# Kernel tuning notes

Hardware: AMD Instinct MI355X
Metric: run time of the kernel (lower is better)

## Reference

```python
import jax, jax.numpy as jnp
import numpy as np

EPS = 1e-5  # torch group_norm default
GROUPS = 32


def _nin(t, W, b):
    # torch Nin: einsum('bchw,co->bowh') transposes spatial dims, then adds bias
    return jnp.einsum('bchw,co->bowh', t, W) + b


def setup_inputs() -> dict:
    key = jax.random.key(0)
    ks = jax.random.split(key, 9)
    B, C, N = 16, 512, 32
    x = jax.random.normal(ks[0], (B, C, N, N), jnp.float32)
    sc = 0.02
    Wq = jax.random.normal(ks[1], (C, C), jnp.float32) * sc
    Wk = jax.random.normal(ks[2], (C, C), jnp.float32) * sc
    Wv = jax.random.normal(ks[3], (C, C), jnp.float32) * sc
    Wn = jax.random.normal(ks[4], (C, C), jnp.float32) * sc
    bq = jnp.zeros((1, C, 1, 1), jnp.float32)
    bk = jnp.zeros((1, C, 1, 1), jnp.float32)
    bv = jnp.zeros((1, C, 1, 1), jnp.float32)
    bn = jnp.zeros((1, C, 1, 1), jnp.float32)
    return {"x": x, "Wq": Wq, "bq": bq, "Wk": Wk, "bk": bk,
            "Wv": Wv, "bv": bv, "Wn": Wn, "bn": bn}


def reference(x, Wq, bq, Wk, bk, Wv, bv, Wn, bn):
    B, C, H, W = x.shape
    # GroupNorm(32) with no affine params
    xg = x.reshape(B, GROUPS, -1)
    mu = xg.mean(-1, keepdims=True)
    var = xg.var(-1, keepdims=True)
    h = ((xg - mu) / jnp.sqrt(var + EPS)).reshape(B, C, H, W)
    # Nin projections -> spatially transposed (B, C, W, H)
    q = _nin(h, Wq, bq)
    k = _nin(h, Wk, bk)
    v = _nin(h, Wv, bv)
    # scores s[b,w1,w2,h1,h2] = sum_c q[b,c,w1,h1] k[b,c,w2,h2] * C^-0.5
    s = jnp.einsum('bcwh,bcWH->bwWhH', q, k) * (C ** -0.5)
    # softmax over flat (h1,h2) blocks exactly as the torch reshape does
    s = jax.nn.softmax(s.reshape(B, H, W, H * W), axis=-1).reshape(B, H, W, H, W)
    # torch.einsum('bHWHW, bcWH -> bcWH', w, v) takes the DIAGONAL over the
    # repeated H and W labels: diag[b,i,j] = s[b,i,j,i,j], then elementwise
    # scales v: out[b,c,w,h] = diag[b,h,w] * v[b,c,w,h]
    i = jnp.arange(H)
    j = jnp.arange(W)
    diag = s[:, i[:, None], j[None, :], i[:, None], j[None, :]]  # (B,H,W)
    h2 = v * jnp.swapaxes(diag, 1, 2)[:, None]  # (B,C,W,H)
    out = _nin(h2, Wn, bn)  # transposes back -> (B,C,H,W)
    return x + out
```

## Files before the change

kernel.cpp:

```cpp
#include <hip/hip_runtime.h>
#include <hip/hip_bf16.h>

typedef __attribute__((ext_vector_type(8))) short short8;
typedef __attribute__((ext_vector_type(4))) float floatx4;

#define MFMA16(a, b, c) __builtin_amdgcn_mfma_f32_16x16x32_bf16((a), (b), (c), 0, 0, 0)

__device__ __forceinline__ short f2bf(float f) {
    union { float f; unsigned u; } x; x.f = f;
    unsigned r = (x.u + 0x7fffu + ((x.u >> 16) & 1u)) >> 16;
    return (short)r;
}
__device__ __forceinline__ float bf2f(short s) {
    union { float f; unsigned u; } x; x.u = ((unsigned)(unsigned short)s) << 16;
    return x.f;
}

__device__ __forceinline__ void gl2lds16(const short* g, short* l) {
    void* gv = const_cast<short*>(g);
    __builtin_amdgcn_global_load_lds((__attribute__((address_space(1))) void*)gv,
                                     (__attribute__((address_space(3))) void*)l,
                                     16, 0, 0);
}

__global__ void transpose_w(const float* __restrict__ Wsrc, short* __restrict__ Wdst) {
    __shared__ float t[32][33];
    int o0 = blockIdx.x * 32, c0 = blockIdx.y * 32;
    int lx = threadIdx.x, ly = threadIdx.y;
    for (int i = ly; i < 32; i += 8) t[i][lx] = Wsrc[(size_t)(c0 + i) * 512 + o0 + lx];
    __syncthreads();
    for (int i = ly; i < 32; i += 8) Wdst[(size_t)(o0 + i) * 512 + c0 + lx] = f2bf(t[lx][i]);
}

__global__ __launch_bounds__(256) void groupnorm_k(const float* __restrict__ x,
                                                   short* __restrict__ hnt) {
    int b = blockIdx.x >> 5, g = blockIdx.x & 31;
    const float* xg = x + ((size_t)b * 512 + g * 16) * 1024;
    const float4* xg4 = (const float4*)xg;
    float s = 0.f, ss = 0.f;
    for (int i = threadIdx.x; i < 4096; i += 256) {
        float4 v = xg4[i];
        s  += v.x + v.y + v.z + v.w;
        ss += v.x * v.x + v.y * v.y + v.z * v.z + v.w * v.w;
    }
#pragma unroll
    for (int off = 32; off > 0; off >>= 1) {
        s  += __shfl_down(s,  off, 64);
        ss += __shfl_down(ss, off, 64);
    }
    __shared__ float red[8];
    int w = threadIdx.x >> 6;
    if ((threadIdx.x & 63) == 0) { red[w] = s; red[4 + w] = ss; }
    __syncthreads();
    float S  = red[0] + red[1] + red[2] + red[3];
    float SS = red[4] + red[5] + red[6] + red[7];
    float mean = S * (1.f / 16384.f);
    float var  = SS * (1.f / 16384.f) - mean * mean;
    float rstd = rsqrtf(var + 1e-5f);
    __shared__ __attribute__((aligned(16))) short tile[16 * 1026];
    for (int i = threadIdx.x; i < 4096; i += 256) {
        float4 v = xg4[i];
        int c = i >> 8, p = (i & 255) * 4;
        short* tp = tile + c * 1026 + p;
        tp[0] = f2bf((v.x - mean) * rstd);
        tp[1] = f2bf((v.y - mean) * rstd);
        tp[2] = f2bf((v.z - mean) * rstd);
        tp[3] = f2bf((v.w - mean) * rstd);
    }
    __syncthreads();
    for (int i = threadIdx.x; i < 2048; i += 256) {
        int p = i >> 1, half = i & 1;
        short8 v;
#pragma unroll
        for (int j = 0; j < 8; ++j) v[j] = tile[(half * 8 + j) * 1026 + p];
        *(short8*)(hnt + ((size_t)b * 1024 + p) * 512 + g * 16 + half * 8) = v;
    }
}

__global__ __launch_bounds__(256) void gemm_nt(const short* __restrict__ A, size_t a_bstride,
                                               const short* __restrict__ W,
                                               const float* __restrict__ bias,
                                               short* __restrict__ Out, size_t o_bstride,
                                               int permute) {
    const int tid = threadIdx.x;
    const int wv = tid >> 6, ln = tid & 63;
    const int m0 = blockIdx.x * 128, n0 = blockIdx.y * 128;
    const short* Ab = A + (size_t)blockIdx.z * a_bstride;
    short* Ob = Out + (size_t)blockIdx.z * o_bstride;

    __shared__ __attribute__((aligned(16))) short As[128 * 32];
    __shared__ __attribute__((aligned(16))) short Bs[128 * 32];

    floatx4 acc[4][4] = {};
    const int wm = (wv >> 1) * 64, wn = (wv & 1) * 64;
    const int fr = ln & 15, fq = ln >> 4;

    for (int kk = 0; kk < 512; kk += 32) {
        __syncthreads();
#pragma unroll
        for (int j = 0; j < 2; ++j) {
            int s = (wv * 2 + j) * 64 + ln;
            int r = s >> 2;
            int q = (s & 3) ^ ((r >> 1) & 3);
            short* lbase = As + (size_t)(wv * 2 + j) * 512;
            gl2lds16(Ab + (size_t)(m0 + r) * 512 + kk + q * 8, lbase);
            short* lbaseB = Bs + (size_t)(wv * 2 + j) * 512;
            gl2lds16(W + (size_t)(n0 + r) * 512 + kk + q * 8, lbaseB);
        }
        __syncthreads();
        short8 af[4], bfr[4];
#pragma unroll
        for (int t = 0; t < 4; ++t) {
            int ra = wm + t * 16 + fr;
            af[t]  = *(const short8*)(As + ra * 32 + ((fq ^ ((ra >> 1) & 3)) * 8));
            int rb = wn + t * 16 + fr;
            bfr[t] = *(const short8*)(Bs + rb * 32 + ((fq ^ ((rb >> 1) & 3)) * 8));
        }
#pragma unroll
        for (int mt = 0; mt < 4; ++mt)
#pragma unroll
            for (int nt = 0; nt < 4; ++nt)
                acc[mt][nt] = MFMA16(af[mt], bfr[nt], acc[mt][nt]);
    }
#pragma unroll
    for (int mt = 0; mt < 4; ++mt) {
#pragma unroll
        for (int nt = 0; nt < 4; ++nt) {
            int n = n0 + wn + nt * 16 + fr;
            float bvv = bias ? bias[n] : 0.0f;
#pragma unroll
            for (int r = 0; r < 4; ++r) {
                int m = m0 + wm + mt * 16 + fq * 4 + r;
                int mrow = permute ? ((m & 31) * 32 + (m >> 5)) : m;
                Ob[(size_t)mrow * 512 + n] = f2bf(acc[mt][nt][r] + bvv);
            }
        }
    }
}

__global__ __launch_bounds__(256) void attn_sm(const short* __restrict__ Qp,
                                               const short* __restrict__ Kp,
                                               float* __restrict__ Dm) {
    const int tid = threadIdx.x;
    const int wv = tid >> 6, ln = tid & 63;
    const int m0 = blockIdx.x * 128, n0 = blockIdx.y * 128, b = blockIdx.z;
    const short* Qb = Qp + (size_t)b * (1024 * 512);
    const short* Kb = Kp + (size_t)b * (1024 * 512);

    __shared__ __attribute__((aligned(16))) short As[128 * 32];
    __shared__ __attribute__((aligned(16))) short Bs[128 * 32];

    floatx4 acc[4][4] = {};
    const int wm = (wv >> 1) * 64, wn = (wv & 1) * 64;
    const int fr = ln & 15, fq = ln >> 4;

    for (int kk = 0; kk < 512; kk += 32) {
        __syncthreads();
#pragma unroll
        for (int j = 0; j < 2; ++j) {
            int s = (wv * 2 + j) * 64 + ln;
            int r = s >> 2;
            int q = (s & 3) ^ ((r >> 1) & 3);
            gl2lds16(Qb + (size_t)(m0 + r) * 512 + kk + q * 8, As + (size_t)(wv * 2 + j) * 512);
            gl2lds16(Kb + (size_t)(n0 + r) * 512 + kk + q * 8, Bs + (size_t)(wv * 2 + j) * 512);
        }
        __syncthreads();
        short8 af[4], bfr[4];
#pragma unroll
        for (int t = 0; t < 4; ++t) {
            int ra = wm + t * 16 + fr;
            af[t]  = *(const short8*)(As + ra * 32 + ((fq ^ ((ra >> 1) & 3)) * 8));
            int rb = wn + t * 16 + fr;
            bfr[t] = *(const short8*)(Bs + rb * 32 + ((fq ^ ((rb >> 1) & 3)) * 8));
        }
#pragma unroll
        for (int mt = 0; mt < 4; ++mt)
#pragma unroll
            for (int nt = 0; nt < 4; ++nt)
                acc[mt][nt] = MFMA16(af[mt], bfr[nt], acc[mt][nt]);
    }

    const float scale = 0.04419417382415922f;
    const int wbase = (m0 + wm) >> 5;
    const int Wbase = (n0 + wn) >> 5;
#pragma unroll
    for (int si = 0; si < 2; ++si) {
#pragma unroll
        for (int sj = 0; sj < 2; ++sj) {
            int wg = wbase + si, Wg = Wbase + sj;
            float tv[16];
            float mx = -3.0e38f;
#pragma unroll
            for (int mi = 0; mi < 2; ++mi)
#pragma unroll
                for (int ni = 0; ni < 2; ++ni)
#pragma unroll
                    for (int r = 0; r < 4; ++r) {
                        float u = acc[2 * si + mi][2 * sj + ni][r] * scale;
                        tv[(mi * 2 + ni) * 4 + r] = u;
                        mx = fmaxf(mx, u);
                    }
#pragma unroll
            for (int off = 32; off > 0; off >>= 1) mx = fmaxf(mx, __shfl_xor(mx, off, 64));
            float se = 0.f;
#pragma unroll
            for (int i = 0; i < 16; ++i) se += __expf(tv[i] - mx);
#pragma unroll
            for (int off = 32; off > 0; off >>= 1) se += __shfl_xor(se, off, 64);
            if (fq == ((wg >> 2) & 3) && fr == (Wg & 15)) {
                int mi = wg >> 4, ni = Wg >> 4;
                float numer = tv[(mi * 2 + ni) * 4 + (wg & 3)];
                Dm[((size_t)b * 32 + wg) * 32 + Wg] = __expf(numer - mx) / se;
            }
        }
    }
}

__global__ __launch_bounds__(256) void epilogue_k(const float* __restrict__ x,
                                                  const short* __restrict__ U,
                                                  const float* __restrict__ Dm,
                                                  const float* __restrict__ bnb,
                                                  float* __restrict__ out) {
    const int tid = threadIdx.x;
    const int b = blockIdx.z, c0 = blockIdx.y * 64, p0 = blockIdx.x * 64;
    __shared__ __attribute__((aligned(16))) short t[64 * 72];
    __shared__ float dsh[64];
#pragma unroll
    for (int j = 0; j < 2; ++j) {
        int ch = j * 256 + tid, r = ch >> 3, q = ch & 7;
        short8 vv = *(const short8*)(U + ((size_t)b * 1024 + p0 + r) * 512 + c0 + q * 8);
        *(short8*)(t + r * 72 + q * 8) = vv;
    }
    if (tid < 64) dsh[tid] = Dm[b * 1024 + p0 + tid];
    __syncthreads();
    for (int e = tid; e < 4096; e += 256) {
        int ci = e >> 6, p = e & 63;
        size_t idx = ((size_t)b * 512 + c0 + ci) * 1024 + p0 + p;
        out[idx] = x[idx] + dsh[p] * bf2f(t[p * 72 + ci]) + bnb[c0 + ci];
    }
}

extern "C" void kernel_launch(void* const* d_in, const int* in_sizes, int n_in,
                              void* d_out, int out_size, void* d_ws, size_t ws_size,
                              hipStream_t stream) {
    const float* x  = (const float*)d_in[0];
    const float* Wq = (const float*)d_in[1];
    const float* bq = (const float*)d_in[2];
    const float* Wk = (const float*)d_in[3];
    const float* bk = (const float*)d_in[4];
    const float* Wv = (const float*)d_in[5];
    const float* bv = (const float*)d_in[6];
    const float* Wn = (const float*)d_in[7];
    const float* bn = (const float*)d_in[8];
    float* out = (float*)d_out;
    char* ws = (char*)d_ws;

    const size_t WSZ = 512 * 512 * 2;
    const size_t TSZ = (size_t)16 * 1024 * 512 * 2;
    short* Wq_t = (short*)(ws);
    short* Wk_t = (short*)(ws + WSZ);
    short* Wv_t = (short*)(ws + 2 * WSZ);
    short* Wn_t = (short*)(ws + 3 * WSZ);
    short* hnt  = (short*)(ws + 4 * WSZ);
    short* Qp   = (short*)(ws + 4 * WSZ + TSZ);
    short* Kp   = (short*)(ws + 4 * WSZ + 2 * TSZ);
    short* Vb   = (short*)(ws + 4 * WSZ + 3 * TSZ);
    float* Dm   = (float*)(ws + 4 * WSZ + 4 * TSZ);
    short* U    = hnt;

    dim3 bt(32, 8);
    transpose_w<<<dim3(16, 16), bt, 0, stream>>>(Wq, Wq_t);
    transpose_w<<<dim3(16, 16), bt, 0, stream>>>(Wk, Wk_t);
    transpose_w<<<dim3(16, 16), bt, 0, stream>>>(Wv, Wv_t);
    transpose_w<<<dim3(16, 16), bt, 0, stream>>>(Wn, Wn_t);
    groupnorm_k<<<512, 256, 0, stream>>>(x, hnt);

    const size_t BS = 1024 * 512;
    gemm_nt<<<dim3(8, 4, 16), 256, 0, stream>>>(hnt, BS, Wq_t, bq, Qp, BS, 1);
    gemm_nt<<<dim3(8, 4, 16), 256, 0, stream>>>(hnt, BS, Wk_t, bk, Kp, BS, 1);
    gemm_nt<<<dim3(8, 4, 16), 256, 0, stream>>>(hnt, BS, Wv_t, bv, Vb, BS, 0);
    attn_sm<<<dim3(8, 8, 16), 256, 0, stream>>>(Qp, Kp, Dm);
    gemm_nt<<<dim3(8, 4, 16), 256, 0, stream>>>(Vb, BS, Wn_t, (const float*)nullptr, U, BS, 0);
    epilogue_k<<<dim3(16, 8, 16), 256, 0, stream>>>(x, U, Dm, bn, out);
}
```

Baseline: 242.0 us.

## Fuse weight transposes, merge QKV GEMMs, widen attention tile, fuse epilogue into output GEMM

Merges the four weight-transpose launches into one launch with a z dimension, and concatenates the Q/K/V weights and biases so a single GEMM launch produces all three projections. The attention-score kernel now uses a 128x256 tile with more accumulators per wave and a launch-bounds occupancy hint. The separate epilogue kernel is removed: the diagonal scale, bias and residual add are applied directly in the output GEMM's register epilogue with float4 stores. This drops the bf16 round-trip through the U buffer and several launches, at the cost of higher register pressure in the attention kernel.

```diff
diff --git a/kernel.cpp b/kernel.cpp
--- a/kernel.cpp
+++ b/kernel.cpp
@@ -10,10 +10,6 @@
     union { float f; unsigned u; } x; x.f = f;
     unsigned r = (x.u + 0x7fffu + ((x.u >> 16) & 1u)) >> 16;
     return (short)r;
-}
-__device__ __forceinline__ float bf2f(short s) {
-    union { float f; unsigned u; } x; x.u = ((unsigned)(unsigned short)s) << 16;
-    return x.f;
 }
 
 __device__ __forceinline__ void gl2lds16(const short* g, short* l) {
@@ -23,13 +19,28 @@
                                      16, 0, 0);
 }
 
-__global__ void transpose_w(const float* __restrict__ Wsrc, short* __restrict__ Wdst) {
+__global__ void transpose_w4(const float* __restrict__ Wq, const float* __restrict__ Wk,
+                             const float* __restrict__ Wv, const float* __restrict__ Wn,
+                             const float* __restrict__ bq, const float* __restrict__ bk,
+                             const float* __restrict__ bv,
+                             short* __restrict__ Wqkv_t, short* __restrict__ Wn_t,
+                             float* __restrict__ bias_cat) {
     __shared__ float t[32][33];
+    int z = blockIdx.z;
+    const float* Wsrc = (z == 0) ? Wq : (z == 1) ? Wk : (z == 2) ? Wv : Wn;
     int o0 = blockIdx.x * 32, c0 = blockIdx.y * 32;
     int lx = threadIdx.x, ly = threadIdx.y;
     for (int i = ly; i < 32; i += 8) t[i][lx] = Wsrc[(size_t)(c0 + i) * 512 + o0 + lx];
     __syncthreads();
-    for (int i = ly; i < 32; i += 8) Wdst[(size_t)(o0 + i) * 512 + c0 + lx] = f2bf(t[lx][i]);
+    for (int i = ly; i < 32; i += 8) {
+        short v = f2bf(t[lx][i]);
+        if (z < 3) Wqkv_t[(size_t)(z * 512 + o0 + i) * 512 + c0 + lx] = v;
+        else       Wn_t[(size_t)(o0 + i) * 512 + c0 + lx] = v;
+    }
+    if (z < 3 && blockIdx.y == 0 && ly == 0) {
+        const float* bsrc = (z == 0) ? bq : (z == 1) ? bk : bv;
+        bias_cat[z * 512 + o0 + lx] = bsrc[o0 + lx];
+    }
 }
 
 __global__ __launch_bounds__(256) void groupnorm_k(const float* __restrict__ x,
@@ -77,16 +88,20 @@
     }
 }
 
-__global__ __launch_bounds__(256) void gemm_nt(const short* __restrict__ A, size_t a_bstride,
-                                               const short* __restrict__ W,
-                                               const float* __restrict__ bias,
-                                               short* __restrict__ Out, size_t o_bstride,
-                                               int permute) {
+__global__ __launch_bounds__(256) void qkv_gemm(const short* __restrict__ A,
+                                                const short* __restrict__ Wt,
+                                                const float* __restrict__ bias_cat,
+                                                short* __restrict__ Qp,
+                                                short* __restrict__ Kp,
+                                                short* __restrict__ Vb) {
     const int tid = threadIdx.x;
     const int wv = tid >> 6, ln = tid & 63;
     const int m0 = blockIdx.x * 128, n0 = blockIdx.y * 128;
-    const short* Ab = A + (size_t)blockIdx.z * a_bstride;
-    short* Ob = Out + (size_t)blockIdx.z * o_bstride;
+    const size_t BS = 1024 * 512;
+    const short* Ab = A + (size_t)blockIdx.z * BS;
+    const int tsel = n0 >> 9;
+    const int permute = (tsel < 2);
+    short* Ob = ((tsel == 0) ? Qp : (tsel == 1) ? Kp : Vb) + (size_t)blockIdx.z * BS;
 
     __shared__ __attribute__((aligned(16))) short As[128 * 32];
     __shared__ __attribute__((aligned(16))) short Bs[128 * 32];
@@ -102,10 +117,8 @@
             int s = (wv * 2 + j) * 64 + ln;
             int r = s >> 2;
             int q = (s & 3) ^ ((r >> 1) & 3);
-            short* lbase = As + (size_t)(wv * 2 + j) * 512;
-            gl2lds16(Ab + (size_t)(m0 + r) * 512 + kk + q * 8, lbase);
-            short* lbaseB = Bs + (size_t)(wv * 2 + j) * 512;
-            gl2lds16(W + (size_t)(n0 + r) * 512 + kk + q * 8, lbaseB);
+            gl2lds16(Ab + (size_t)(m0 + r) * 512 + kk + q * 8, As + (size_t)(wv * 2 + j) * 512);
+            gl2lds16(Wt + (size_t)(n0 + r) * 512 + kk + q * 8, Bs + (size_t)(wv * 2 + j) * 512);
         }
         __syncthreads();
         short8 af[4], bfr[4];
@@ -127,31 +140,32 @@
 #pragma unroll
         for (int nt = 0; nt < 4; ++nt) {
             int n = n0 + wn + nt * 16 + fr;
-            float bvv = bias ? bias[n] : 0.0f;
+            float bvv = bias_cat[n];
+            int nn = n & 511;
 #pragma unroll
             for (int r = 0; r < 4; ++r) {
                 int m = m0 + wm + mt * 16 + fq * 4 + r;
                 int mrow = permute ? ((m & 31) * 32 + (m >> 5)) : m;
-                Ob[(size_t)mrow * 512 + n] = f2bf(acc[mt][nt][r] + bvv);
+                Ob[(size_t)mrow * 512 + nn] = f2bf(acc[mt][nt][r] + bvv);
             }
         }
     }
 }
 
-__global__ __launch_bounds__(256) void attn_sm(const short* __restrict__ Qp,
-                                               const short* __restrict__ Kp,
-                                               float* __restrict__ Dm) {
+__global__ __launch_bounds__(256, 2) void attn_sm(const short* __restrict__ Qp,
+                                                  const short* __restrict__ Kp,
+                                                  float* __restrict__ Dm) {
     const int tid = threadIdx.x;
     const int wv = tid >> 6, ln = tid & 63;
-    const int m0 = blockIdx.x * 128, n0 = blockIdx.y * 128, b = blockIdx.z;
+    const int m0 = blockIdx.x * 128, n0 = blockIdx.y * 256, b = blockIdx.z;
     const short* Qb = Qp + (size_t)b * (1024 * 512);
     const short* Kb = Kp + (size_t)b * (1024 * 512);
 
     __shared__ __attribute__((aligned(16))) short As[128 * 32];
-    __shared__ __attribute__((aligned(16))) short Bs[128 * 32];
-
-    floatx4 acc[4][4] = {};
-    const int wm = (wv >> 1) * 64, wn = (wv & 1) * 64;
+    __shared__ __attribute__((aligned(16))) short Bs[256 * 32];
+
+    floatx4 acc[4][8] = {};
+    const int wm = (wv >> 1) * 64, wn = (wv & 1) * 128;
     const int fr = ln & 15, fq = ln >> 4;
 
     for (int kk = 0; kk < 512; kk += 32) {
@@ -162,21 +176,30 @@
             int r = s >> 2;
             int q = (s & 3) ^ ((r >> 1) & 3);
             gl2lds16(Qb + (size_t)(m0 + r) * 512 + kk + q * 8, As + (size_t)(wv * 2 + j) * 512);
-            gl2lds16(Kb + (size_t)(n0 + r) * 512 + kk + q * 8, Bs + (size_t)(wv * 2 + j) * 512);
-        }
-        __syncthreads();
-        short8 af[4], bfr[4];
+        }
+#pragma unroll
+        for (int j = 0; j < 4; ++j) {
+            int s = (wv * 4 + j) * 64 + ln;
+            int r = s >> 2;
+            int q = (s & 3) ^ ((r >> 1) & 3);
+            gl2lds16(Kb + (size_t)(n0 + r) * 512 + kk + q * 8, Bs + (size_t)(wv * 4 + j) * 512);
+        }
+        __syncthreads();
+        short8 af[4], bfr[8];
 #pragma unroll
         for (int t = 0; t < 4; ++t) {
             int ra = wm + t * 16 + fr;
-            af[t]  = *(const short8*)(As + ra * 32 + ((fq ^ ((ra >> 1) & 3)) * 8));
-            int rb = wn + t * 16 + fr;
-            bfr[t] = *(const short8*)(Bs + rb * 32 + ((fq ^ ((rb >> 1) & 3)) * 8));
+            af[t] = *(const short8*)(As + ra * 32 + ((fq ^ ((ra >> 1) & 3)) * 8));
+        }
+#pragma unroll
+        for (int u = 0; u < 8; ++u) {
+            int rb = wn + u * 16 + fr;
+            bfr[u] = *(const short8*)(Bs + rb * 32 + ((fq ^ ((rb >> 1) & 3)) * 8));
         }
 #pragma unroll
         for (int mt = 0; mt < 4; ++mt)
 #pragma unroll
-            for (int nt = 0; nt < 4; ++nt)
+            for (int nt = 0; nt < 8; ++nt)
                 acc[mt][nt] = MFMA16(af[mt], bfr[nt], acc[mt][nt]);
     }
 
@@ -186,7 +209,7 @@
 #pragma unroll
     for (int si = 0; si < 2; ++si) {
 #pragma unroll
-        for (int sj = 0; sj < 2; ++sj) {
+        for (int sj = 0; sj < 4; ++sj) {
             int wg = wbase + si, Wg = Wbase + sj;
             float tv[16];
             float mx = -3.0e38f;
@@ -216,27 +239,67 @@
     }
 }
 
-__global__ __launch_bounds__(256) void epilogue_k(const float* __restrict__ x,
-                                                  const short* __restrict__ U,
-                                                  const float* __restrict__ Dm,
-                                                  const float* __restrict__ bnb,
-                                                  float* __restrict__ out) {
+__global__ __launch_bounds__(256) void out_gemm(const short* __restrict__ A,
+                                                const short* __restrict__ Wt,
+                                                const float* __restrict__ Dm,
+                                                const float* __restrict__ bnb,
+                                                const float* __restrict__ x,
+                                                float* __restrict__ out) {
     const int tid = threadIdx.x;
-    const int b = blockIdx.z, c0 = blockIdx.y * 64, p0 = blockIdx.x * 64;
-    __shared__ __attribute__((aligned(16))) short t[64 * 72];
-    __shared__ float dsh[64];
-#pragma unroll
-    for (int j = 0; j < 2; ++j) {
-        int ch = j * 256 + tid, r = ch >> 3, q = ch & 7;
-        short8 vv = *(const short8*)(U + ((size_t)b * 1024 + p0 + r) * 512 + c0 + q * 8);
-        *(short8*)(t + r * 72 + q * 8) = vv;
-    }
-    if (tid < 64) dsh[tid] = Dm[b * 1024 + p0 + tid];
-    __syncthreads();
-    for (int e = tid; e < 4096; e += 256) {
-        int ci = e >> 6, p = e & 63;
-        size_t idx = ((size_t)b * 512 + c0 + ci) * 1024 + p0 + p;
-        out[idx] = x[idx] + dsh[p] * bf2f(t[p * 72 + ci]) + bnb[c0 + ci];
+    const int wv = tid >> 6, ln = tid & 63;
+    const int m0 = blockIdx.x * 128, n0 = blockIdx.y * 128, b = blockIdx.z;
+    const size_t BS = 1024 * 512;
+    const short* Ab = A + (size_t)b * BS;
+
+    __shared__ __attribute__((aligned(16))) short As[128 * 32];
+    __shared__ __attribute__((aligned(16))) short Bs[128 * 32];
+
+    floatx4 acc[4][4] = {};
+    const int wm = (wv >> 1) * 64, wn = (wv & 1) * 64;
+    const int fr = ln & 15, fq = ln >> 4;
+
+    for (int kk = 0; kk < 512; kk += 32) {
+        __syncthreads();
+#pragma unroll
+        for (int j = 0; j < 2; ++j) {
+            int s = (wv * 2 + j) * 64 + ln;
+            int r = s >> 2;
+            int q = (s & 3) ^ ((r >> 1) & 3);
+            gl2lds16(Ab + (size_t)(m0 + r) * 512 + kk + q * 8, As + (size_t)(wv * 2 + j) * 512);
+            gl2lds16(Wt + (size_t)(n0 + r) * 512 + kk + q * 8, Bs + (size_t)(wv * 2 + j) * 512);
+        }
+        __syncthreads();
+        short8 af[4], bfr[4];
+#pragma unroll
+        for (int t = 0; t < 4; ++t) {
+            int ra = wm + t * 16 + fr;
+            af[t]  = *(const short8*)(As + ra * 32 + ((fq ^ ((ra >> 1) & 3)) * 8));
+            int rb = wn + t * 16 + fr;
+            bfr[t] = *(const short8*)(Bs + rb * 32 + ((fq ^ ((rb >> 1) & 3)) * 8));
+        }
+#pragma unroll
+        for (int mt = 0; mt < 4; ++mt)
+#pragma unroll
+            for (int nt = 0; nt < 4; ++nt)
+                acc[mt][nt] = MFMA16(af[mt], bfr[nt], acc[mt][nt]);
+    }
+#pragma unroll
+    for (int mt = 0; mt < 4; ++mt) {
+        int mbase = m0 + wm + mt * 16 + fq * 4;
+        float4 d4 = *(const float4*)(Dm + (size_t)b * 1024 + mbase);
+#pragma unroll
+        for (int nt = 0; nt < 4; ++nt) {
+            int n = n0 + wn + nt * 16 + fr;
+            float bvv = bnb[n];
+            size_t base = ((size_t)b * 512 + n) * 1024 + mbase;
+            float4 x4 = *(const float4*)(x + base);
+            float4 o;
+            o.x = x4.x + d4.x * acc[mt][nt][0] + bvv;
+            o.y = x4.y + d4.y * acc[mt][nt][1] + bvv;
+            o.z = x4.z + d4.z * acc[mt][nt][2] + bvv;
+            o.w = x4.w + d4.w * acc[mt][nt][3] + bvv;
+            *(float4*)(out + base) = o;
+        }
     }
 }
 
@@ -255,31 +318,24 @@
     float* out = (float*)d_out;
     char* ws = (char*)d_ws;
 
-    const size_t WSZ = 512 * 512 * 2;
-    const size_t TSZ = (size_t)16 * 1024 * 512 * 2;
-    short* Wq_t = (short*)(ws);
-    short* Wk_t = (short*)(ws + WSZ);
-    short* Wv_t = (short*)(ws + 2 * WSZ);
-    short* Wn_t = (short*)(ws + 3 * WSZ);
-    short* hnt  = (short*)(ws + 4 * WSZ);
-    short* Qp   = (short*)(ws + 4 * WSZ + TSZ);
-    short* Kp   = (short*)(ws + 4 * WSZ + 2 * TSZ);
-    short* Vb   = (short*)(ws + 4 * WSZ + 3 * TSZ);
-    float* Dm   = (float*)(ws + 4 * WSZ + 4 * TSZ);
-    short* U    = hnt;
-
-    dim3 bt(32, 8);
-    transpose_w<<<dim3(16, 16), bt, 0, stream>>>(Wq, Wq_t);
-    transpose_w<<<dim3(16, 16), bt, 0, stream>>>(Wk, Wk_t);
-    transpose_w<<<dim3(16, 16), bt, 0, stream>>>(Wv, Wv_t);
-    transpose_w<<<dim3(16, 16), bt, 0, stream>>>(Wn, Wn_t);
+    const size_t WQKV = (size_t)1536 * 512 * 2;
+    const size_t WSZ  = (size_t)512 * 512 * 2;
+    const size_t BIAS = 1536 * sizeof(float);
+    const size_t TSZ  = (size_t)16 * 1024 * 512 * 2;
+    short* Wqkv_t   = (short*)(ws);
+    short* Wn_t     = (short*)(ws + WQKV);
+    float* bias_cat = (float*)(ws + WQKV + WSZ);
+    char*  base     = ws + WQKV + WSZ + BIAS;
+    short* hnt = (short*)(base);
+    short* Qp  = (short*)(base + TSZ);
+    short* Kp  = (short*)(base + 2 * TSZ);
+    short* Vb  = (short*)(base + 3 * TSZ);
+    float* Dm  = (float*)(base + 4 * TSZ);
+
+    transpose_w4<<<dim3(16, 16, 4), dim3(32, 8), 0, stream>>>(
+        Wq, Wk, Wv, Wn, bq, bk, bv, Wqkv_t, Wn_t, bias_cat);
     groupnorm_k<<<512, 256, 0, stream>>>(x, hnt);
-
-    const size_t BS = 1024 * 512;
-    gemm_nt<<<dim3(8, 4, 16), 256, 0, stream>>>(hnt, BS, Wq_t, bq, Qp, BS, 1);
-    gemm_nt<<<dim3(8, 4, 16), 256, 0, stream>>>(hnt, BS, Wk_t, bk, Kp, BS, 1);
-    gemm_nt<<<dim3(8, 4, 16), 256, 0, stream>>>(hnt, BS, Wv_t, bv, Vb, BS, 0);
-    attn_sm<<<dim3(8, 8, 16), 256, 0, stream>>>(Qp, Kp, Dm);
-    gemm_nt<<<dim3(8, 4, 16), 256, 0, stream>>>(Vb, BS, Wn_t, (const float*)nullptr, U, BS, 0);
-    epilogue_k<<<dim3(16, 8, 16), 256, 0, stream>>>(x, U, Dm, bn, out);
-}
+    qkv_gemm<<<dim3(8, 12, 16), 256, 0, stream>>>(hnt, Wqkv_t, bias_cat, Qp, Kp, Vb);
+    attn_sm<<<dim3(8, 4, 16), 256, 0, stream>>>(Qp, Kp, Dm);
+    out_gemm<<<dim3(8, 4, 16), 256, 0, stream>>>(Vb, Wn_t, Dm, bn, x, out);
+}
```

New measurement: 213.0 us. -12.0%, faster.
